# Optimization experiments

Hardware: AMD Instinct MI355X
Metric: run time of the kernel (lower is better)

Reference implementation:

```python
import jax, jax.numpy as jnp
import numpy as np

B, S, D = 4, 2048, 1024
H = 16
HD = D // H

def setup_inputs() -> dict:
    key = jax.random.key(0)
    ks = jax.random.split(key, 6)
    scale = 1.0 / np.sqrt(D)
    x = jax.random.normal(ks[0], (B, S, D), dtype=jnp.float32)
    Wq = jax.random.normal(ks[1], (D, D), dtype=jnp.float32) * scale
    Wk = jax.random.normal(ks[2], (D, D), dtype=jnp.float32) * scale
    Wv = jax.random.normal(ks[3], (D, D), dtype=jnp.float32) * scale
    Wo = jax.random.normal(ks[4], (D, D), dtype=jnp.float32) * scale
    bo = jax.random.normal(ks[5], (D,), dtype=jnp.float32) * 0.01
    return {"x": x, "Wq": Wq, "Wk": Wk, "Wv": Wv, "Wo": Wo, "bo": bo}

def reference(x, Wq, Wk, Wv, Wo, bo):
    b, n, _ = x.shape
    # QKV projections (no bias), split into heads: [b, h, n, hd]
    q = (x @ Wq).reshape(b, n, H, HD).transpose(0, 2, 1, 3)
    k = (x @ Wk).reshape(b, n, H, HD).transpose(0, 2, 1, 3)
    v = (x @ Wv).reshape(b, n, H, HD).transpose(0, 2, 1, 3)
    scores = jnp.einsum('bhqd,bhkd->bhqk', q, k) / jnp.sqrt(jnp.float32(HD))
    causal = jnp.tril(jnp.ones((n, n), dtype=bool))
    scores = jnp.where(causal, scores, -jnp.inf)
    attn = jax.nn.softmax(scores, axis=-1)  # dropout p=0.0 -> identity
    ctx = jnp.einsum('bhqk,bhkd->bhqd', attn, v)
    ctx = ctx.transpose(0, 2, 1, 3).reshape(b, n, D)
    return ctx @ Wo + bo
```

## Files before the change

kernel.cpp:

```cpp
#include <hip/hip_runtime.h>

#define S_   2048
#define D_   1024
#define H_   16
#define HD_  64
#define NTOK 8192
#define QKS  2048
#define QSCALE 0.18033688f

typedef __attribute__((ext_vector_type(8))) __bf16 bf16x8;
typedef __attribute__((ext_vector_type(4))) float  f32x4;

#define GPTR(p) ((__attribute__((address_space(1))) void*)(unsigned long long)(p))
#define LPTR(p) ((__attribute__((address_space(3))) void*)(p))

__global__ __launch_bounds__(256) void k_prep(const float* __restrict__ x,
                                              __bf16* __restrict__ xb,
                                              const float* __restrict__ Wq,
                                              const float* __restrict__ Wk,
                                              const float* __restrict__ Wv,
                                              const float* __restrict__ Wo,
                                              __bf16* __restrict__ wqkt,
                                              __bf16* __restrict__ wvt,
                                              __bf16* __restrict__ wot) {
    const int bx = blockIdx.x;
    if (bx < 4096) {
        int i = bx * 2048 + threadIdx.x * 8;
        f32x4 a = *(const f32x4*)(x + i);
        f32x4 b = *(const f32x4*)(x + i + 4);
        bf16x8 o;
#pragma unroll
        for (int j = 0; j < 4; j++) { o[j] = (__bf16)a[j]; o[4 + j] = (__bf16)b[j]; }
        *(bf16x8*)(xb + i) = o;
        return;
    }
    __shared__ float t[32][33];
    const int tt = bx - 4096;
    const int widx = tt >> 10, r = tt & 1023;
    const float* W;
    __bf16* Wt;
    switch (widx) {
        case 0: W = Wq; Wt = wqkt; break;
        case 1: W = Wk; Wt = wqkt + (size_t)D_ * D_; break;
        case 2: W = Wv; Wt = wvt; break;
        default: W = Wo; Wt = wot; break;
    }
    const int i0 = (r & 31) * 32, j0 = (r >> 5) * 32;
    const int tx = threadIdx.x & 31, ty = threadIdx.x >> 5;
#pragma unroll
    for (int rr = 0; rr < 32; rr += 8)
        t[ty + rr][tx] = W[(size_t)(i0 + ty + rr) * D_ + j0 + tx];
    __syncthreads();
#pragma unroll
    for (int rr = 0; rr < 32; rr += 8)
        Wt[(size_t)(j0 + ty + rr) * D_ + i0 + tx] = (__bf16)t[tx][ty + rr];
}

__device__ __forceinline__ void gemm_body_bf16(const __bf16* __restrict__ A,
                                               const __bf16* __restrict__ Bt,
                                               __bf16* __restrict__ C,
                                               int N, int K, int tm, int tn,
                                               float scale,
                                               __bf16* As, __bf16* Bs) {
    const int tid  = threadIdx.x;
    const int wave = tid >> 6, lane = tid & 63;
    const int quad = lane >> 4, l16 = lane & 15;
    const int wm = (wave & 1) * 64, wn = (wave >> 1) * 64;
    f32x4 acc[4][4] = {};

    for (int k0 = 0; k0 < K; k0 += 32) {
        __syncthreads();
#pragma unroll
        for (int s = 0; s < 2; s++) {
            const int cb = s * 256 + wave * 64;
            const int c  = cb + lane;
            const int row = c >> 2, kc = (c & 3) * 8;
            __builtin_amdgcn_global_load_lds(GPTR(A + (size_t)(tm + row) * K + k0 + kc),
                                             LPTR(As + cb * 8), 16, 0, 0);
            __builtin_amdgcn_global_load_lds(GPTR(Bt + (size_t)(tn + row) * K + k0 + kc),
                                             LPTR(Bs + cb * 8), 16, 0, 0);
        }
        __syncthreads();

        bf16x8 af[4], bf[4];
#pragma unroll
        for (int mi = 0; mi < 4; mi++)
            af[mi] = *(const bf16x8*)&As[(wm + mi * 16 + l16) * 32 + quad * 8];
#pragma unroll
        for (int ni = 0; ni < 4; ni++)
            bf[ni] = *(const bf16x8*)&Bs[(wn + ni * 16 + l16) * 32 + quad * 8];
#pragma unroll
        for (int mi = 0; mi < 4; mi++)
#pragma unroll
            for (int ni = 0; ni < 4; ni++)
                acc[mi][ni] = __builtin_amdgcn_mfma_f32_16x16x32_bf16(
                    af[mi], bf[ni], acc[mi][ni], 0, 0, 0);
    }

#pragma unroll
    for (int mi = 0; mi < 4; mi++)
#pragma unroll
        for (int ni = 0; ni < 4; ni++)
#pragma unroll
            for (int r = 0; r < 4; r++) {
                const int row = tm + wm + mi * 16 + quad * 4 + r;
                const int col = tn + wn + ni * 16 + l16;
                C[(size_t)row * N + col] = (__bf16)(acc[mi][ni][r] * scale);
            }
}

__global__ __launch_bounds__(256) void k_gemm_qkv(const __bf16* __restrict__ xb,
                                                  const __bf16* __restrict__ wqkt,
                                                  const __bf16* __restrict__ wvt,
                                                  __bf16* __restrict__ qk,
                                                  __bf16* __restrict__ VT) {
    __shared__ __bf16 As[128 * 32];
    __shared__ __bf16 Bs[128 * 32];
    const int bx = blockIdx.x;
    if (bx < 1024) {
        const int tm = (bx & 63) * 128, tn = (bx >> 6) * 128;
        const float scale = (tn < D_) ? QSCALE : 1.0f;
        gemm_body_bf16(xb, wqkt, qk, QKS, D_, tm, tn, scale, As, Bs);
    } else {
        const int b2 = bx - 1024;
        const int tm = (b2 & 7) * 128, tn = (b2 >> 3) * 128;
        gemm_body_bf16(wvt, xb, VT, NTOK, D_, tm, tn, 1.0f, As, Bs);
    }
}

__global__ __launch_bounds__(256) void k_gemm_o(const __bf16* __restrict__ A,
                                                const __bf16* __restrict__ Bt,
                                                float* __restrict__ C,
                                                const float* __restrict__ bias) {
    __shared__ __bf16 As[128 * 32];
    __shared__ __bf16 Bs[128 * 32];
    const int tid  = threadIdx.x;
    const int wave = tid >> 6, lane = tid & 63;
    const int quad = lane >> 4, l16 = lane & 15;
    const int tm = blockIdx.x * 128, tn = blockIdx.y * 128;
    const int wm = (wave & 1) * 64, wn = (wave >> 1) * 64;
    const int N = D_, K = D_;
    f32x4 acc[4][4] = {};

    for (int k0 = 0; k0 < K; k0 += 32) {
        __syncthreads();
#pragma unroll
        for (int s = 0; s < 2; s++) {
            const int cb = s * 256 + wave * 64;
            const int c  = cb + lane;
            const int row = c >> 2, kc = (c & 3) * 8;
            __builtin_amdgcn_global_load_lds(GPTR(A + (size_t)(tm + row) * K + k0 + kc),
                                             LPTR(As + cb * 8), 16, 0, 0);
            __builtin_amdgcn_global_load_lds(GPTR(Bt + (size_t)(tn + row) * K + k0 + kc),
                                             LPTR(Bs + cb * 8), 16, 0, 0);
        }
        __syncthreads();

        bf16x8 af[4], bf[4];
#pragma unroll
        for (int mi = 0; mi < 4; mi++)
            af[mi] = *(const bf16x8*)&As[(wm + mi * 16 + l16) * 32 + quad * 8];
#pragma unroll
        for (int ni = 0; ni < 4; ni++)
            bf[ni] = *(const bf16x8*)&Bs[(wn + ni * 16 + l16) * 32 + quad * 8];
#pragma unroll
        for (int mi = 0; mi < 4; mi++)
#pragma unroll
            for (int ni = 0; ni < 4; ni++)
                acc[mi][ni] = __builtin_amdgcn_mfma_f32_16x16x32_bf16(
                    af[mi], bf[ni], acc[mi][ni], 0, 0, 0);
    }

#pragma unroll
    for (int mi = 0; mi < 4; mi++)
#pragma unroll
        for (int ni = 0; ni < 4; ni++)
#pragma unroll
            for (int r = 0; r < 4; r++) {
                const int row = tm + wm + mi * 16 + quad * 4 + r;
                const int col = tn + wn + ni * 16 + l16;
                C[(size_t)row * N + col] = acc[mi][ni][r] + bias[col];
            }
}

__global__ __launch_bounds__(256) void k_attn(const __bf16* __restrict__ Qb,
                                              const __bf16* __restrict__ Kb,
                                              const __bf16* __restrict__ VT,
                                              __bf16* __restrict__ ctx) {
    __shared__ __bf16 Ks[2][64 * 64];
    __shared__ __bf16 Vs[2][64 * 64];
    __shared__ __bf16 P[4][32 * 72];

    const int tid = threadIdx.x;
    const int wave = tid >> 6, lane = tid & 63;
    const int quad = lane >> 4, l16 = lane & 15;
    const int h = blockIdx.y, b = blockIdx.z;
    const size_t tok0 = (size_t)b * S_;
    const size_t hoff = (size_t)h * HD_;

    bf16x8 onesv;
#pragma unroll
    for (int j = 0; j < 8; j++) onesv[j] = (__bf16)1.0f;

    auto stage = [&](int kv, int buf) {
#pragma unroll
        for (int s = 0; s < 2; s++) {
            const int cb = s * 256 + wave * 64;
            const int c  = cb + lane;
            const int row = c >> 3;
            const int gc  = (c & 7) ^ (row & 7);
            __builtin_amdgcn_global_load_lds(
                GPTR(Kb + (size_t)(tok0 + kv + row) * QKS + hoff + gc * 8),
                LPTR(&Ks[buf][cb * 8]), 16, 0, 0);
            __builtin_amdgcn_global_load_lds(
                GPTR(VT + (hoff + row) * (size_t)NTOK + tok0 + kv + gc * 8),
                LPTR(&Vs[buf][cb * 8]), 16, 0, 0);
        }
    };

#pragma unroll 1
    for (int sidx = 0; sidx < 2; sidx++) {
        const int qt = sidx == 0 ? blockIdx.x : 15 - blockIdx.x;
        const int qb = qt * 128;
        const int q0 = qb + wave * 32;

        bf16x8 qf[2][2];
#pragma unroll
        for (int qi = 0; qi < 2; qi++)
#pragma unroll
            for (int ks = 0; ks < 2; ks++)
                qf[qi][ks] = *(const bf16x8*)&Qb[(tok0 + q0 + qi * 16 + l16) * QKS +
                                                 hoff + ks * 32 + quad * 8];

        f32x4 oacc[2][4] = {};
        f32x4 lacc[2] = {};
        const int ktb = (qb + 127) >> 6;

        stage(0, 0);
        __syncthreads();

        for (int kt = 0; kt <= ktb; kt++) {
            const int cur = kt & 1;
            const int kv0 = kt * 64;
            if (kt < ktb) stage(kv0 + 64, 1 - cur);

            if (kv0 <= q0 + 31) {
                f32x4 sacc[2][4] = {};
#pragma unroll
                for (int ks = 0; ks < 2; ks++)
#pragma unroll
                    for (int ksub = 0; ksub < 4; ksub++) {
                        const int r = ksub * 16 + l16;
                        bf16x8 kf = *(const bf16x8*)
                            &Ks[cur][(r * 8 + (((ks * 4 + quad) ^ (r & 7)))) * 8];
#pragma unroll
                        for (int qi = 0; qi < 2; qi++)
                            sacc[qi][ksub] = __builtin_amdgcn_mfma_f32_16x16x32_bf16(
                                qf[qi][ks], kf, sacc[qi][ksub], 0, 0, 0);
                    }
                if (kv0 + 63 > q0) {
#pragma unroll
                    for (int qi = 0; qi < 2; qi++)
#pragma unroll
                        for (int ksub = 0; ksub < 4; ksub++)
#pragma unroll
                            for (int r = 0; r < 4; r++) {
                                const int kg = kv0 + ksub * 16 + l16;
                                const int qg = q0 + qi * 16 + quad * 4 + r;
                                if (kg > qg) sacc[qi][ksub][r] = -1e30f;
                            }
                }
#pragma unroll
                for (int qi = 0; qi < 2; qi++)
#pragma unroll
                    for (int ksub = 0; ksub < 4; ksub++)
#pragma unroll
                        for (int r = 0; r < 4; r++)
                            P[wave][(qi * 16 + quad * 4 + r) * 72 + ksub * 16 + l16] =
                                (__bf16)__builtin_amdgcn_exp2f(sacc[qi][ksub][r]);
                asm volatile("s_waitcnt lgkmcnt(0)" ::: "memory");
#pragma unroll
                for (int ks2 = 0; ks2 < 2; ks2++) {
                    bf16x8 af[2];
#pragma unroll
                    for (int qi = 0; qi < 2; qi++)
                        af[qi] = *(const bf16x8*)&P[wave][(qi * 16 + l16) * 72 +
                                                          ks2 * 32 + quad * 8];
#pragma unroll
                    for (int qi = 0; qi < 2; qi++)
                        lacc[qi] = __builtin_amdgcn_mfma_f32_16x16x32_bf16(
                            af[qi], onesv, lacc[qi], 0, 0, 0);
#pragma unroll
                    for (int hs = 0; hs < 4; hs++) {
                        const int row = hs * 16 + l16;
                        bf16x8 vf = *(const bf16x8*)
                            &Vs[cur][(row * 8 + (((ks2 * 4 + quad) ^ (row & 7)))) * 8];
#pragma unroll
                        for (int qi = 0; qi < 2; qi++)
                            oacc[qi][hs] = __builtin_amdgcn_mfma_f32_16x16x32_bf16(
                                af[qi], vf, oacc[qi][hs], 0, 0, 0);
                    }
                }
            }
            __syncthreads();
        }

#pragma unroll
        for (int qi = 0; qi < 2; qi++) {
            f32x4 rl;
#pragma unroll
            for (int r = 0; r < 4; r++) rl[r] = 1.0f / lacc[qi][r];
#pragma unroll
            for (int hs = 0; hs < 4; hs++)
#pragma unroll
                for (int r = 0; r < 4; r++) {
                    const int qg = q0 + qi * 16 + quad * 4 + r;
                    ctx[(tok0 + qg) * D_ + hoff + hs * 16 + l16] =
                        (__bf16)(oacc[qi][hs][r] * rl[r]);
                }
        }
    }
}

extern "C" void kernel_launch(void* const* d_in, const int* in_sizes, int n_in,
                              void* d_out, int out_size, void* d_ws, size_t ws_size,
                              hipStream_t stream) {
    const float* x  = (const float*)d_in[0];
    const float* Wq = (const float*)d_in[1];
    const float* Wk = (const float*)d_in[2];
    const float* Wv = (const float*)d_in[3];
    const float* Wo = (const float*)d_in[4];
    const float* bo = (const float*)d_in[5];
    float* out = (float*)d_out;

    char* p = (char*)d_ws;
    __bf16* xb   = (__bf16*)p; p += (size_t)NTOK * D_ * 2;
    __bf16* wqkt = (__bf16*)p; p += (size_t)2 * D_ * D_ * 2;
    __bf16* wvt  = (__bf16*)p; p += (size_t)D_ * D_ * 2;
    __bf16* wot  = (__bf16*)p; p += (size_t)D_ * D_ * 2;
    __bf16* qk   = (__bf16*)p; p += (size_t)NTOK * QKS * 2;
    __bf16* VT   = (__bf16*)p; p += (size_t)NTOK * D_ * 2;
    __bf16* ctx  = (__bf16*)p; p += (size_t)NTOK * D_ * 2;

    k_prep<<<dim3(4096 + 4 * 1024), 256, 0, stream>>>(x, xb, Wq, Wk, Wv, Wo,
                                                      wqkt, wvt, wot);
    k_gemm_qkv<<<dim3(1024 + 512), 256, 0, stream>>>(xb, wqkt, wvt, qk, VT);
    k_attn<<<dim3(8, H_, 4), 256, 0, stream>>>(qk, qk + D_, VT, ctx);
    k_gemm_o<<<dim3(64, 8), 256, 0, stream>>>(ctx, wot, out, bo);
}
```

Before: 258.3 us.

## Restructure attention to 2-wave blocks with 64 query rows per wave

The attention kernel moves from 4-wave blocks, each handling a paired light and heavy query tile, to 2-wave blocks that each own one 128-row query tile, launching twice as many blocks with the heaviest tiles first. Each wave now covers 64 query rows, so every K/V tile staged in shared memory is reused across more MFMAs, and the diagonal mask only runs on exactly aligned tiles. The aim is higher arithmetic intensity per LDS load plus finer-grained scheduling. In exchange, register pressure per wave grows (accumulators double), and load balance now depends on the block scheduler rather than on explicit tile pairing.

```diff
diff --git a/kernel.cpp b/kernel.cpp
--- a/kernel.cpp
+++ b/kernel.cpp
@@ -183,13 +183,13 @@
             }
 }
 
-__global__ __launch_bounds__(256) void k_attn(const __bf16* __restrict__ Qb,
-                                              const __bf16* __restrict__ Kb,
-                                              const __bf16* __restrict__ VT,
-                                              __bf16* __restrict__ ctx) {
+__global__ __launch_bounds__(128, 2) void k_attn(const __bf16* __restrict__ Qb,
+                                                 const __bf16* __restrict__ Kb,
+                                                 const __bf16* __restrict__ VT,
+                                                 __bf16* __restrict__ ctx) {
     __shared__ __bf16 Ks[2][64 * 64];
     __shared__ __bf16 Vs[2][64 * 64];
-    __shared__ __bf16 P[4][32 * 72];
+    __shared__ __bf16 P[2][64 * 72];
 
     const int tid = threadIdx.x;
     const int wave = tid >> 6, lane = tid & 63;
@@ -198,14 +198,18 @@
     const size_t tok0 = (size_t)b * S_;
     const size_t hoff = (size_t)h * HD_;
 
+    const int qt = 15 - blockIdx.x;
+    const int qb = qt * 128;
+    const int q0 = qb + wave * 64;
+
     bf16x8 onesv;
 #pragma unroll
     for (int j = 0; j < 8; j++) onesv[j] = (__bf16)1.0f;
 
     auto stage = [&](int kv, int buf) {
 #pragma unroll
-        for (int s = 0; s < 2; s++) {
-            const int cb = s * 256 + wave * 64;
+        for (int s = 0; s < 4; s++) {
+            const int cb = s * 128 + wave * 64;
             const int c  = cb + lane;
             const int row = c >> 3;
             const int gc  = (c & 7) ^ (row & 7);
@@ -218,107 +222,100 @@
         }
     };
 
-#pragma unroll 1
-    for (int sidx = 0; sidx < 2; sidx++) {
-        const int qt = sidx == 0 ? blockIdx.x : 15 - blockIdx.x;
-        const int qb = qt * 128;
-        const int q0 = qb + wave * 32;
-
-        bf16x8 qf[2][2];
-#pragma unroll
-        for (int qi = 0; qi < 2; qi++)
-#pragma unroll
-            for (int ks = 0; ks < 2; ks++)
-                qf[qi][ks] = *(const bf16x8*)&Qb[(tok0 + q0 + qi * 16 + l16) * QKS +
-                                                 hoff + ks * 32 + quad * 8];
-
-        f32x4 oacc[2][4] = {};
-        f32x4 lacc[2] = {};
-        const int ktb = (qb + 127) >> 6;
-
-        stage(0, 0);
-        __syncthreads();
-
-        for (int kt = 0; kt <= ktb; kt++) {
-            const int cur = kt & 1;
-            const int kv0 = kt * 64;
-            if (kt < ktb) stage(kv0 + 64, 1 - cur);
-
-            if (kv0 <= q0 + 31) {
-                f32x4 sacc[2][4] = {};
-#pragma unroll
-                for (int ks = 0; ks < 2; ks++)
-#pragma unroll
-                    for (int ksub = 0; ksub < 4; ksub++) {
-                        const int r = ksub * 16 + l16;
-                        bf16x8 kf = *(const bf16x8*)
-                            &Ks[cur][(r * 8 + (((ks * 4 + quad) ^ (r & 7)))) * 8];
-#pragma unroll
-                        for (int qi = 0; qi < 2; qi++)
-                            sacc[qi][ksub] = __builtin_amdgcn_mfma_f32_16x16x32_bf16(
-                                qf[qi][ks], kf, sacc[qi][ksub], 0, 0, 0);
-                    }
-                if (kv0 + 63 > q0) {
-#pragma unroll
-                    for (int qi = 0; qi < 2; qi++)
-#pragma unroll
-                        for (int ksub = 0; ksub < 4; ksub++)
-#pragma unroll
-                            for (int r = 0; r < 4; r++) {
-                                const int kg = kv0 + ksub * 16 + l16;
-                                const int qg = q0 + qi * 16 + quad * 4 + r;
-                                if (kg > qg) sacc[qi][ksub][r] = -1e30f;
-                            }
+    bf16x8 qf[4][2];
+#pragma unroll
+    for (int qi = 0; qi < 4; qi++)
+#pragma unroll
+        for (int ks = 0; ks < 2; ks++)
+            qf[qi][ks] = *(const bf16x8*)&Qb[(tok0 + q0 + qi * 16 + l16) * QKS +
+                                             hoff + ks * 32 + quad * 8];
+
+    f32x4 oacc[4][4] = {};
+    f32x4 lacc[4] = {};
+    const int ktb = 2 * qt + 1;
+
+    stage(0, 0);
+    __syncthreads();
+
+    for (int kt = 0; kt <= ktb; kt++) {
+        const int cur = kt & 1;
+        const int kv0 = kt * 64;
+        if (kt < ktb) stage(kv0 + 64, 1 - cur);
+
+        if (kv0 <= q0) {
+            const bool diag = (kv0 == q0);
+#pragma unroll
+            for (int ksub = 0; ksub < 4; ksub++) {
+                const int krow = ksub * 16 + l16;
+                bf16x8 kf0 = *(const bf16x8*)
+                    &Ks[cur][(krow * 8 + ((quad) ^ (krow & 7))) * 8];
+                bf16x8 kf1 = *(const bf16x8*)
+                    &Ks[cur][(krow * 8 + ((4 + quad) ^ (krow & 7))) * 8];
+                f32x4 s[4];
+#pragma unroll
+                for (int qi = 0; qi < 4; qi++) {
+                    s[qi] = __builtin_amdgcn_mfma_f32_16x16x32_bf16(
+                        qf[qi][0], kf0, (f32x4){0.f, 0.f, 0.f, 0.f}, 0, 0, 0);
+                    s[qi] = __builtin_amdgcn_mfma_f32_16x16x32_bf16(
+                        qf[qi][1], kf1, s[qi], 0, 0, 0);
                 }
-#pragma unroll
-                for (int qi = 0; qi < 2; qi++)
-#pragma unroll
-                    for (int ksub = 0; ksub < 4; ksub++)
-#pragma unroll
-                        for (int r = 0; r < 4; r++)
-                            P[wave][(qi * 16 + quad * 4 + r) * 72 + ksub * 16 + l16] =
-                                (__bf16)__builtin_amdgcn_exp2f(sacc[qi][ksub][r]);
-                asm volatile("s_waitcnt lgkmcnt(0)" ::: "memory");
-#pragma unroll
-                for (int ks2 = 0; ks2 < 2; ks2++) {
-                    bf16x8 af[2];
-#pragma unroll
-                    for (int qi = 0; qi < 2; qi++)
-                        af[qi] = *(const bf16x8*)&P[wave][(qi * 16 + l16) * 72 +
-                                                          ks2 * 32 + quad * 8];
-#pragma unroll
-                    for (int qi = 0; qi < 2; qi++)
-                        lacc[qi] = __builtin_amdgcn_mfma_f32_16x16x32_bf16(
-                            af[qi], onesv, lacc[qi], 0, 0, 0);
-#pragma unroll
-                    for (int hs = 0; hs < 4; hs++) {
-                        const int row = hs * 16 + l16;
-                        bf16x8 vf = *(const bf16x8*)
-                            &Vs[cur][(row * 8 + (((ks2 * 4 + quad) ^ (row & 7)))) * 8];
-#pragma unroll
-                        for (int qi = 0; qi < 2; qi++)
-                            oacc[qi][hs] = __builtin_amdgcn_mfma_f32_16x16x32_bf16(
-                                af[qi], vf, oacc[qi][hs], 0, 0, 0);
-                    }
+                if (diag) {
+#pragma unroll
+                    for (int qi = 0; qi < 4; qi++)
+#pragma unroll
+                        for (int r = 0; r < 4; r++) {
+                            const int kg = kv0 + krow;
+                            const int qg = q0 + qi * 16 + quad * 4 + r;
+                            if (kg > qg) s[qi][r] = -1e30f;
+                        }
                 }
-            }
-            __syncthreads();
+#pragma unroll
+                for (int qi = 0; qi < 4; qi++)
+#pragma unroll
+                    for (int r = 0; r < 4; r++)
+                        P[wave][(qi * 16 + quad * 4 + r) * 72 + krow] =
+                            (__bf16)__builtin_amdgcn_exp2f(s[qi][r]);
+            }
+            asm volatile("s_waitcnt lgkmcnt(0)" ::: "memory");
+#pragma unroll
+            for (int ks2 = 0; ks2 < 2; ks2++) {
+                bf16x8 af[4];
+#pragma unroll
+                for (int qi = 0; qi < 4; qi++)
+                    af[qi] = *(const bf16x8*)&P[wave][(qi * 16 + l16) * 72 +
+                                                      ks2 * 32 + quad * 8];
+#pragma unroll
+                for (int qi = 0; qi < 4; qi++)
+                    lacc[qi] = __builtin_amdgcn_mfma_f32_16x16x32_bf16(
+                        af[qi], onesv, lacc[qi], 0, 0, 0);
+#pragma unroll
+                for (int hs = 0; hs < 4; hs++) {
+                    const int row = hs * 16 + l16;
+                    bf16x8 vf = *(const bf16x8*)
+                        &Vs[cur][(row * 8 + (((ks2 * 4 + quad) ^ (row & 7)))) * 8];
+#pragma unroll
+                    for (int qi = 0; qi < 4; qi++)
+                        oacc[qi][hs] = __builtin_amdgcn_mfma_f32_16x16x32_bf16(
+                            af[qi], vf, oacc[qi][hs], 0, 0, 0);
+                }
+            }
         }
-
-#pragma unroll
-        for (int qi = 0; qi < 2; qi++) {
-            f32x4 rl;
-#pragma unroll
-            for (int r = 0; r < 4; r++) rl[r] = 1.0f / lacc[qi][r];
-#pragma unroll
-            for (int hs = 0; hs < 4; hs++)
-#pragma unroll
-                for (int r = 0; r < 4; r++) {
-                    const int qg = q0 + qi * 16 + quad * 4 + r;
-                    ctx[(tok0 + qg) * D_ + hoff + hs * 16 + l16] =
-                        (__bf16)(oacc[qi][hs][r] * rl[r]);
-                }
-        }
+        __syncthreads();
+    }
+
+#pragma unroll
+    for (int qi = 0; qi < 4; qi++) {
+        f32x4 rl;
+#pragma unroll
+        for (int r = 0; r < 4; r++) rl[r] = 1.0f / lacc[qi][r];
+#pragma unroll
+        for (int hs = 0; hs < 4; hs++)
+#pragma unroll
+            for (int r = 0; r < 4; r++) {
+                const int qg = q0 + qi * 16 + quad * 4 + r;
+                ctx[(tok0 + qg) * D_ + hoff + hs * 16 + l16] =
+                    (__bf16)(oacc[qi][hs][r] * rl[r]);
+            }
     }
 }
 
@@ -345,6 +342,6 @@
     k_prep<<<dim3(4096 + 4 * 1024), 256, 0, stream>>>(x, xb, Wq, Wk, Wv, Wo,
                                                       wqkt, wvt, wot);
     k_gemm_qkv<<<dim3(1024 + 512), 256, 0, stream>>>(xb, wqkt, wvt, qk, VT);
-    k_attn<<<dim3(8, H_, 4), 256, 0, stream>>>(qk, qk + D_, VT, ctx);
+    k_attn<<<dim3(16, H_, 4), 128, 0, stream>>>(qk, qk + D_, VT, ctx);
     k_gemm_o<<<dim3(64, 8), 256, 0, stream>>>(ctx, wot, out, bo);
 }
```

New measurement: 332.3 us. 28.7% more time.

## Keep softmax probabilities in registers via transposed score MFMA, drop LDS P buffer

Applied to the files above, without the earlier changes.

Computes the score tile transposed (K as A operand) so each lane's exp'd probabilities directly form the B operand of a 16x16x16 bf16 MFMA for P·V. This removes the per-wave LDS round trip for P and the ones-vector MFMA for row sums, which are now accumulated in registers and reduced with cross-lane shuffles. Output stores become 4-wide vectors. It also adds a launch-bounds occupancy hint of 2, trading register headroom for occupancy, and uses the smaller-K MFMA, which issues more instructions for P·V.

```diff
diff --git a/kernel.cpp b/kernel.cpp
--- a/kernel.cpp
+++ b/kernel.cpp
@@ -9,7 +9,9 @@
 #define QSCALE 0.18033688f
 
 typedef __attribute__((ext_vector_type(8))) __bf16 bf16x8;
+typedef __attribute__((ext_vector_type(4))) __bf16 bf16x4;
 typedef __attribute__((ext_vector_type(4))) float  f32x4;
+typedef __attribute__((ext_vector_type(4))) short  short4v;
 
 #define GPTR(p) ((__attribute__((address_space(1))) void*)(unsigned long long)(p))
 #define LPTR(p) ((__attribute__((address_space(3))) void*)(p))
@@ -183,13 +185,17 @@
             }
 }
 
-__global__ __launch_bounds__(256) void k_attn(const __bf16* __restrict__ Qb,
-                                              const __bf16* __restrict__ Kb,
-                                              const __bf16* __restrict__ VT,
-                                              __bf16* __restrict__ ctx) {
+__device__ __forceinline__ short bf16_bits(float f) {
+    __bf16 h = (__bf16)f;
+    return __builtin_bit_cast(short, h);
+}
+
+__global__ __launch_bounds__(256, 2) void k_attn(const __bf16* __restrict__ Qb,
+                                                 const __bf16* __restrict__ Kb,
+                                                 const __bf16* __restrict__ VT,
+                                                 __bf16* __restrict__ ctx) {
     __shared__ __bf16 Ks[2][64 * 64];
     __shared__ __bf16 Vs[2][64 * 64];
-    __shared__ __bf16 P[4][32 * 72];
 
     const int tid = threadIdx.x;
     const int wave = tid >> 6, lane = tid & 63;
@@ -197,10 +203,6 @@
     const int h = blockIdx.y, b = blockIdx.z;
     const size_t tok0 = (size_t)b * S_;
     const size_t hoff = (size_t)h * HD_;
-
-    bf16x8 onesv;
-#pragma unroll
-    for (int j = 0; j < 8; j++) onesv[j] = (__bf16)1.0f;
 
     auto stage = [&](int kv, int buf) {
 #pragma unroll
@@ -233,7 +235,7 @@
                                                  hoff + ks * 32 + quad * 8];
 
         f32x4 oacc[2][4] = {};
-        f32x4 lacc[2] = {};
+        float lsum[2] = {0.f, 0.f};
         const int ktb = (qb + 127) >> 6;
 
         stage(0, 0);
@@ -245,7 +247,7 @@
             if (kt < ktb) stage(kv0 + 64, 1 - cur);
 
             if (kv0 <= q0 + 31) {
-                f32x4 sacc[2][4] = {};
+                f32x4 st[2][4] = {};
 #pragma unroll
                 for (int ks = 0; ks < 2; ks++)
 #pragma unroll
@@ -255,8 +257,8 @@
                             &Ks[cur][(r * 8 + (((ks * 4 + quad) ^ (r & 7)))) * 8];
 #pragma unroll
                         for (int qi = 0; qi < 2; qi++)
-                            sacc[qi][ksub] = __builtin_amdgcn_mfma_f32_16x16x32_bf16(
-                                qf[qi][ks], kf, sacc[qi][ksub], 0, 0, 0);
+                            st[qi][ksub] = __builtin_amdgcn_mfma_f32_16x16x32_bf16(
+                                kf, qf[qi][ks], st[qi][ksub], 0, 0, 0);
                     }
                 if (kv0 + 63 > q0) {
 #pragma unroll
@@ -265,59 +267,56 @@
                         for (int ksub = 0; ksub < 4; ksub++)
 #pragma unroll
                             for (int r = 0; r < 4; r++) {
-                                const int kg = kv0 + ksub * 16 + l16;
-                                const int qg = q0 + qi * 16 + quad * 4 + r;
-                                if (kg > qg) sacc[qi][ksub][r] = -1e30f;
+                                const int kg = kv0 + ksub * 16 + quad * 4 + r;
+                                const int qg = q0 + qi * 16 + l16;
+                                if (kg > qg) st[qi][ksub][r] = -1e30f;
                             }
                 }
+                short4v pfrag[2][4];
 #pragma unroll
                 for (int qi = 0; qi < 2; qi++)
 #pragma unroll
-                    for (int ksub = 0; ksub < 4; ksub++)
-#pragma unroll
-                        for (int r = 0; r < 4; r++)
-                            P[wave][(qi * 16 + quad * 4 + r) * 72 + ksub * 16 + l16] =
-                                (__bf16)__builtin_amdgcn_exp2f(sacc[qi][ksub][r]);
-                asm volatile("s_waitcnt lgkmcnt(0)" ::: "memory");
-#pragma unroll
-                for (int ks2 = 0; ks2 < 2; ks2++) {
-                    bf16x8 af[2];
-#pragma unroll
-                    for (int qi = 0; qi < 2; qi++)
-                        af[qi] = *(const bf16x8*)&P[wave][(qi * 16 + l16) * 72 +
-                                                          ks2 * 32 + quad * 8];
-#pragma unroll
-                    for (int qi = 0; qi < 2; qi++)
-                        lacc[qi] = __builtin_amdgcn_mfma_f32_16x16x32_bf16(
-                            af[qi], onesv, lacc[qi], 0, 0, 0);
+                    for (int ksub = 0; ksub < 4; ksub++) {
+                        float p0 = __builtin_amdgcn_exp2f(st[qi][ksub][0]);
+                        float p1 = __builtin_amdgcn_exp2f(st[qi][ksub][1]);
+                        float p2 = __builtin_amdgcn_exp2f(st[qi][ksub][2]);
+                        float p3 = __builtin_amdgcn_exp2f(st[qi][ksub][3]);
+                        lsum[qi] += (p0 + p1) + (p2 + p3);
+                        short4v pf = {bf16_bits(p0), bf16_bits(p1),
+                                      bf16_bits(p2), bf16_bits(p3)};
+                        pfrag[qi][ksub] = pf;
+                    }
+#pragma unroll
+                for (int ksub = 0; ksub < 4; ksub++)
 #pragma unroll
                     for (int hs = 0; hs < 4; hs++) {
                         const int row = hs * 16 + l16;
-                        bf16x8 vf = *(const bf16x8*)
-                            &Vs[cur][(row * 8 + (((ks2 * 4 + quad) ^ (row & 7)))) * 8];
+                        const int swz = (ksub * 2 + (quad >> 1)) ^ (row & 7);
+                        short4v vf = *(const short4v*)
+                            &Vs[cur][row * 64 + swz * 8 + (quad & 1) * 4];
 #pragma unroll
                         for (int qi = 0; qi < 2; qi++)
-                            oacc[qi][hs] = __builtin_amdgcn_mfma_f32_16x16x32_bf16(
-                                af[qi], vf, oacc[qi][hs], 0, 0, 0);
+                            oacc[qi][hs] = __builtin_amdgcn_mfma_f32_16x16x16bf16_1k(
+                                vf, pfrag[qi][ksub], oacc[qi][hs], 0, 0, 0);
                     }
-                }
             }
             __syncthreads();
         }
 
 #pragma unroll
         for (int qi = 0; qi < 2; qi++) {
-            f32x4 rl;
-#pragma unroll
-            for (int r = 0; r < 4; r++) rl[r] = 1.0f / lacc[qi][r];
-#pragma unroll
-            for (int hs = 0; hs < 4; hs++)
-#pragma unroll
-                for (int r = 0; r < 4; r++) {
-                    const int qg = q0 + qi * 16 + quad * 4 + r;
-                    ctx[(tok0 + qg) * D_ + hoff + hs * 16 + l16] =
-                        (__bf16)(oacc[qi][hs][r] * rl[r]);
-                }
+            float v = lsum[qi];
+            v += __shfl_xor(v, 16);
+            v += __shfl_xor(v, 32);
+            const float rl = 1.0f / v;
+#pragma unroll
+            for (int hs = 0; hs < 4; hs++) {
+                bf16x4 o;
+#pragma unroll
+                for (int r = 0; r < 4; r++) o[r] = (__bf16)(oacc[qi][hs][r] * rl);
+                *(bf16x4*)&ctx[(tok0 + q0 + qi * 16 + l16) * D_ + hoff +
+                               hs * 16 + quad * 4] = o;
+            }
         }
     }
 }
```

New measurement: 250.8 us. -2.9%, faster.
